# Kernel optimization log

Measured on AMD Instinct MI355X. Metric: run time of the kernel, lower is better.

The kernel has to match this reference:

```python
import jax, jax.numpy as jnp
import numpy as np

N = 32768        # nodes
E = 524288       # edges (avg degree 16)
F_NODE = 64      # NODE_FEATURE_DIM
H = 128          # GNN_HIDDEN
F_EDGE = 32      # EDGE_FEATURE_DIM
L = 3            # GNN_LAYERS
D = 256          # D_MODEL
B = 64           # graphs per batch
MAXN = N // B    # 512 nodes per graph (equal-size for static to_dense_batch)


def setup_inputs() -> dict:
    key = jax.random.key(0)
    ks = jax.random.split(key, 10)
    p = lambda k, shape: jax.random.normal(k, shape, jnp.float32) * 0.02
    return {
        "x": jax.random.normal(ks[0], (N, F_NODE), jnp.float32),
        "edge_attr": jax.random.normal(ks[1], (E, F_EDGE), jnp.float32),
        "node_emb_w": p(ks[2], (F_NODE, H)), "node_emb_b": jnp.zeros((H,), jnp.float32),
        "msg_w1": p(ks[3], (L, 2 * H + F_EDGE, 2 * H)), "msg_b1": jnp.zeros((L, 2 * H), jnp.float32),
        "msg_w2": p(ks[4], (L, 2 * H, H)), "msg_b2": jnp.zeros((L, H), jnp.float32),
        "upd_w": p(ks[5], (L, 2 * H, H)), "upd_b": jnp.zeros((L, H), jnp.float32),
        "upd_ln_g": jnp.ones((L, H), jnp.float32), "upd_ln_b": jnp.zeros((L, H), jnp.float32),
        "norm_g": jnp.ones((L, H), jnp.float32), "norm_b": jnp.zeros((L, H), jnp.float32),
        "proj_w": p(ks[6], (H, D)), "proj_b": jnp.zeros((D,), jnp.float32),
        "edge_index": jax.random.randint(ks[7], (2, E), 0, N),
        "batch": jnp.arange(N, dtype=jnp.int32) // MAXN,  # sorted, 64 graphs of 512
    }


def layer_norm(x, g, b, eps=1e-5):
    m = x.mean(-1, keepdims=True)
    v = ((x - m) ** 2).mean(-1, keepdims=True)
    return (x - m) * jax.lax.rsqrt(v + eps) * g + b


def reference(x, edge_attr, node_emb_w, node_emb_b, msg_w1, msg_b1, msg_w2, msg_b2,
              upd_w, upd_b, upd_ln_g, upd_ln_b, norm_g, norm_b, proj_w, proj_b,
              edge_index, batch):
    src, dst = edge_index[0], edge_index[1]  # PyG: x_j = x[src], x_i = x[dst]
    h = x @ node_emb_w + node_emb_b          # [N, H]
    n_layers = msg_w1.shape[0]
    for l in range(n_layers):
        # message: gather -> concat -> MLP (dropout inactive at eval)
        m = jnp.concatenate([h[dst], h[src], edge_attr], axis=-1)  # [E, 2H+Fe]
        m = jax.nn.relu(m @ msg_w1[l] + msg_b1[l])
        m = m @ msg_w2[l] + msg_b2[l]                               # [E, H]
        # aggregate: scatter-add over destination nodes
        aggr = jax.ops.segment_sum(m, dst, num_segments=h.shape[0])  # [N, H]
        # update: concat -> Linear -> ReLU -> LayerNorm
        u = jnp.concatenate([h, aggr], axis=-1) @ upd_w[l] + upd_b[l]
        u = layer_norm(jax.nn.relu(u), upd_ln_g[l], upd_ln_b[l])
        # residual + outer LayerNorm
        h = layer_norm(h + u, norm_g[l], norm_b[l])
    # to_dense_batch (batch sorted, equal-size graphs -> static [B, MAXN])
    n = h.shape[0]
    counts = jax.ops.segment_sum(jnp.ones((n,), jnp.int32), batch, num_segments=B)
    starts = jnp.concatenate([jnp.zeros((1,), jnp.int32), jnp.cumsum(counts)[:-1]])
    pos = jnp.arange(n, dtype=jnp.int32) - starts[batch]
    dense = jnp.zeros((B, MAXN, h.shape[-1]), h.dtype).at[batch, pos].set(h)
    mask = jnp.zeros((B, MAXN), bool).at[batch, pos].set(True)
    return dense @ proj_w + proj_b, mask
```

## Files before the change

### kernel.cpp

```cpp
#include <hip/hip_runtime.h>

#define NN 32768
#define NE 524288

typedef __attribute__((ext_vector_type(8))) short bf16x8;
typedef __attribute__((ext_vector_type(4))) float f32x4;

__device__ __forceinline__ unsigned short f2bf(float f) {
  unsigned int u = __float_as_uint(f);
  unsigned int r = (u + 0x7FFFu + ((u >> 16) & 1u)) >> 16;
  return (unsigned short)r;
}
__device__ __forceinline__ float bf2f(unsigned short s) {
  return __uint_as_float(((unsigned int)s) << 16);
}

__device__ __forceinline__ void lds_fence_wave() {
  asm volatile("s_waitcnt lgkmcnt(0)" ::: "memory");
  __builtin_amdgcn_sched_barrier(0);
}

__global__ void prep_frag_kernel(const float* __restrict__ W, int row0, int ldw, long lstrW,
                                 unsigned short* __restrict__ out, int outOff, int outLstr,
                                 int K, int N, int total) {
  int t = blockIdx.x * 256 + threadIdx.x;
  if (t >= total) return;
  int lane = t & 63, fi = t >> 6;
  int FR = (K >> 5) * (N >> 4);
  int l = fi / FR; fi -= l * FR;
  int NT = N >> 4;
  int nt = fi % NT, kc = fi / NT;
  int i = lane & 15, g = lane >> 4;
  const float* base = W + (long)l * lstrW;
  bf16x8 v;
#pragma unroll
  for (int j = 0; j < 8; ++j)
    v[j] = (short)f2bf(base[(long)(row0 + kc * 32 + g * 8 + j) * ldw + nt * 16 + i]);
  reinterpret_cast<bf16x8*>(out)[(long)(l * outLstr + outOff + fi) * 64 + lane] = v;
}

__global__ void wcomp_kernel(const float* __restrict__ W2, const float* __restrict__ Wu,
                             float* __restrict__ out) {
  int t = blockIdx.x * 256 + threadIdx.x;
  if (t >= 3 * 256 * 128) return;
  int c = t & 127, a = (t >> 7) & 255, l = t >> 15;
  const float* w2 = W2 + (long)l * 32768 + a * 128;
  const float* wu = Wu + (long)l * 32768 + 128 * 128 + c;
  float s = 0.f;
#pragma unroll 8
  for (int j = 0; j < 128; ++j) s += w2[j] * wu[j * 128];
  out[t] = s;
}

__global__ void c2_kernel(const float* __restrict__ b2, const float* __restrict__ Wu,
                          float* __restrict__ out) {
  int t = blockIdx.x * 256 + threadIdx.x;
  if (t >= 3 * 128) return;
  int c = t & 127, l = t >> 7;
  const float* bb = b2 + l * 128;
  const float* wu = Wu + (long)l * 32768 + 128 * 128 + c;
  float s = 0.f;
#pragma unroll 8
  for (int j = 0; j < 128; ++j) s += bb[j] * wu[j * 128];
  out[t] = s;
}

__global__ void hist_kernel(const int* __restrict__ eidx, int* __restrict__ deg) {
  int t = blockIdx.x * 256 + threadIdx.x;
  if (t < NE) atomicAdd(&deg[eidx[NE + t]], 1);
}

__global__ void scan_kernel(const int* __restrict__ deg, int* __restrict__ cursor,
                            float* __restrict__ degf) {
  __shared__ int lds[1024];
  int t = threadIdx.x;
  int vals[32];
  int s = 0;
#pragma unroll
  for (int j = 0; j < 32; ++j) {
    int d = deg[t * 32 + j];
    vals[j] = d; s += d;
    degf[t * 32 + j] = (float)d;
  }
  lds[t] = s;
  __syncthreads();
  for (int off = 1; off < 1024; off <<= 1) {
    int tmp = 0;
    if (t >= off) tmp = lds[t - off];
    __syncthreads();
    lds[t] += tmp;
    __syncthreads();
  }
  int run = lds[t] - s;
#pragma unroll
  for (int j = 0; j < 32; ++j) { cursor[t * 32 + j] = run; run += vals[j]; }
}

__global__ void scatter_kernel(const int* __restrict__ eidx, const float* __restrict__ ea,
                               int* __restrict__ cursor,
                               int* __restrict__ dsts, int* __restrict__ srcs,
                               unsigned short* __restrict__ ea_s) {
  int t = blockIdx.x * 256 + threadIdx.x;
  if (t >= NE) return;
  int d = eidx[NE + t], s = eidx[t];
  int pos = atomicAdd(&cursor[d], 1);
  dsts[pos] = d;
  srcs[pos] = s;
  const float4* ep = reinterpret_cast<const float4*>(ea + (long)t * 32);
  unsigned short* op = ea_s + (long)pos * 32;
#pragma unroll
  for (int q = 0; q < 4; ++q) {
    float4 f0 = ep[2 * q], f1 = ep[2 * q + 1];
    bf16x8 v;
    v[0] = (short)f2bf(f0.x); v[1] = (short)f2bf(f0.y);
    v[2] = (short)f2bf(f0.z); v[3] = (short)f2bf(f0.w);
    v[4] = (short)f2bf(f1.x); v[5] = (short)f2bf(f1.y);
    v[6] = (short)f2bf(f1.z); v[7] = (short)f2bf(f1.w);
    *reinterpret_cast<bf16x8*>(op + q * 8) = v;
  }
}

__global__ __launch_bounds__(256, 2)
void node_emb_kernel(const float* __restrict__ x,
                     const unsigned short* __restrict__ wf,
                     const float* __restrict__ bias,
                     unsigned short* __restrict__ h_bf,
                     float* __restrict__ h_f32) {
  int tid = threadIdx.x, lane = tid & 63, w = tid >> 6;
  int i = lane & 15, g = lane >> 4;
  int nbase = blockIdx.x * 64 + w * 16;
  f32x4 zero = {0.f, 0.f, 0.f, 0.f};
  f32x4 acc[8];
#pragma unroll
  for (int nt = 0; nt < 8; ++nt) acc[nt] = zero;
#pragma unroll
  for (int kc = 0; kc < 2; ++kc) {
    const float* xp = x + (nbase + i) * 64 + kc * 32 + g * 8;
    float4 f0 = *reinterpret_cast<const float4*>(xp);
    float4 f1 = *reinterpret_cast<const float4*>(xp + 4);
    bf16x8 af;
    af[0] = (short)f2bf(f0.x); af[1] = (short)f2bf(f0.y);
    af[2] = (short)f2bf(f0.z); af[3] = (short)f2bf(f0.w);
    af[4] = (short)f2bf(f1.x); af[5] = (short)f2bf(f1.y);
    af[6] = (short)f2bf(f1.z); af[7] = (short)f2bf(f1.w);
#pragma unroll
    for (int nt = 0; nt < 8; ++nt) {
      bf16x8 bf = reinterpret_cast<const bf16x8*>(wf)[(kc * 8 + nt) * 64 + lane];
      acc[nt] = __builtin_amdgcn_mfma_f32_16x16x32_bf16(af, bf, acc[nt], 0, 0, 0);
    }
  }
#pragma unroll
  for (int nt = 0; nt < 8; ++nt) {
    int c = nt * 16 + i;
    float b = bias[c];
#pragma unroll
    for (int r = 0; r < 4; ++r) {
      int node = nbase + 4 * g + r;
      float v = acc[nt][r] + b;
      h_f32[node * 128 + c] = v;
      h_bf[node * 128 + c] = f2bf(v);
    }
  }
}

__global__ __launch_bounds__(256, 2)
void pq_kernel(const unsigned short* __restrict__ h_bf,
               const unsigned short* __restrict__ wfa,
               const unsigned short* __restrict__ wfb,
               const float* __restrict__ b1,
               unsigned short* __restrict__ P, unsigned short* __restrict__ Q,
               float* __restrict__ haggr) {
  int tid = threadIdx.x, lane = tid & 63, w = tid >> 6;
  int i = lane & 15, g = lane >> 4;
  int nbase = blockIdx.x * 64 + w * 16;
  {
    const float4 zz = make_float4(0.f, 0.f, 0.f, 0.f);
    float4* hz = reinterpret_cast<float4*>(haggr + (long)blockIdx.x * 64 * 256);
#pragma unroll
    for (int it = 0; it < 16; ++it) hz[tid + 256 * it] = zz;
  }
  f32x4 zero = {0.f, 0.f, 0.f, 0.f};
  f32x4 accP[16], accQ[16];
#pragma unroll
  for (int nt = 0; nt < 16; ++nt) { accP[nt] = zero; accQ[nt] = zero; }
#pragma unroll
  for (int kc = 0; kc < 4; ++kc) {
    bf16x8 af = *reinterpret_cast<const bf16x8*>(h_bf + (nbase + i) * 128 + kc * 32 + g * 8);
#pragma unroll
    for (int nt = 0; nt < 16; ++nt) {
      bf16x8 ba = reinterpret_cast<const bf16x8*>(wfa)[(kc * 16 + nt) * 64 + lane];
      accP[nt] = __builtin_amdgcn_mfma_f32_16x16x32_bf16(af, ba, accP[nt], 0, 0, 0);
      bf16x8 bb = reinterpret_cast<const bf16x8*>(wfb)[(kc * 16 + nt) * 64 + lane];
      accQ[nt] = __builtin_amdgcn_mfma_f32_16x16x32_bf16(af, bb, accQ[nt], 0, 0, 0);
    }
  }
#pragma unroll
  for (int nt = 0; nt < 16; ++nt) {
    int c = nt * 16 + i;
    float b = b1[c];
#pragma unroll
    for (int r = 0; r < 4; ++r) {
      int node = nbase + 4 * g + r;
      P[(long)node * 256 + c] = f2bf(accP[nt][r] + b);
      Q[(long)node * 256 + c] = f2bf(accQ[nt][r]);
    }
  }
}

#define RP 264
__global__ __launch_bounds__(128, 4)
void edge_kernel5(const unsigned short* __restrict__ P,
                  const unsigned short* __restrict__ Q,
                  const int* __restrict__ dsts, const int* __restrict__ srcs,
                  const unsigned short* __restrict__ ea_s,
                  const unsigned short* __restrict__ w1cf,
                  float* __restrict__ haggr) {
  __shared__ unsigned short R[32 * RP];
  __shared__ float xch[2][256];
  const int tid = threadIdx.x;
  const int lane = tid & 63, w = tid >> 6;
  const int i = lane & 15, g = lane >> 4;
  const int p0 = blockIdx.x * 32;
  const int kb = w * 16;

  int dvs[16], svs[16];
#pragma unroll
  for (int k = 0; k < 16; ++k) {
    dvs[k] = __builtin_amdgcn_readfirstlane(dsts[p0 + kb + k]);
    svs[k] = __builtin_amdgcn_readfirstlane(srcs[p0 + kb + k]);
  }

  {
    bf16x8 bfrag = *reinterpret_cast<const bf16x8*>(ea_s + (long)(p0 + kb + i) * 32 + g * 8);
    f32x4 zero = {0.f, 0.f, 0.f, 0.f};
    f32x4 acc[16];
#pragma unroll
    for (int m = 0; m < 16; ++m) acc[m] = zero;
#pragma unroll
    for (int m = 0; m < 16; ++m) {
      bf16x8 afrag = reinterpret_cast<const bf16x8*>(w1cf)[m * 64 + lane];
      acc[m] = __builtin_amdgcn_mfma_f32_16x16x32_bf16(afrag, bfrag, acc[m], 0, 0, 0);
    }
#pragma unroll
    for (int m = 0; m < 16; ++m) {
      union { unsigned short s[4]; unsigned long long u; } pk;
#pragma unroll
      for (int r = 0; r < 4; ++r) pk.s[r] = f2bf(acc[m][r]);
      *reinterpret_cast<unsigned long long*>(&R[(kb + i) * RP + m * 16 + 4 * g]) = pk.u;
    }
  }

  const int c4 = lane * 4;
  ushort4 qv[16];
#pragma unroll
  for (int k = 0; k < 16; ++k)
    qv[k] = *reinterpret_cast<const ushort4*>(Q + (long)svs[k] * 256 + c4);
  float pf[4];
  int dvPrev = dvs[0];
  {
    ushort4 pv = *reinterpret_cast<const ushort4*>(P + (long)dvPrev * 256 + c4);
    pf[0] = bf2f(pv.x); pf[1] = bf2f(pv.y); pf[2] = bf2f(pv.z); pf[3] = bf2f(pv.w);
  }

  lds_fence_wave();

  float acc4[4] = {0.f, 0.f, 0.f, 0.f};
#pragma unroll
  for (int k = 0; k < 16; ++k) {
    int dv = dvs[k];
    if (dv != dvPrev) {
      *reinterpret_cast<float4*>(&xch[w][c4]) = make_float4(acc4[0], acc4[1], acc4[2], acc4[3]);
      lds_fence_wave();
      float* hp = haggr + (long)dvPrev * 256;
#pragma unroll
      for (int j = 0; j < 4; ++j) atomicAdd(hp + lane + 64 * j, xch[w][lane + 64 * j]);
      acc4[0] = acc4[1] = acc4[2] = acc4[3] = 0.f;
      ushort4 pv = *reinterpret_cast<const ushort4*>(P + (long)dv * 256 + c4);
      pf[0] = bf2f(pv.x); pf[1] = bf2f(pv.y); pf[2] = bf2f(pv.z); pf[3] = bf2f(pv.w);
      dvPrev = dv;
    }
    ushort4 rv = *reinterpret_cast<const ushort4*>(&R[(kb + k) * RP + c4]);
    float v0 = pf[0] + bf2f(qv[k].x) + bf2f(rv.x);
    float v1 = pf[1] + bf2f(qv[k].y) + bf2f(rv.y);
    float v2 = pf[2] + bf2f(qv[k].z) + bf2f(rv.z);
    float v3 = pf[3] + bf2f(qv[k].w) + bf2f(rv.w);
    acc4[0] += v0 > 0.f ? v0 : 0.f;
    acc4[1] += v1 > 0.f ? v1 : 0.f;
    acc4[2] += v2 > 0.f ? v2 : 0.f;
    acc4[3] += v3 > 0.f ? v3 : 0.f;
  }
  {
    *reinterpret_cast<float4*>(&xch[w][c4]) = make_float4(acc4[0], acc4[1], acc4[2], acc4[3]);
    lds_fence_wave();
    float* hp = haggr + (long)dvPrev * 256;
#pragma unroll
    for (int j = 0; j < 4; ++j) atomicAdd(hp + lane + 64 * j, xch[w][lane + 64 * j]);
  }
}

__global__ __launch_bounds__(256, 2)
void upd_kernel2(const unsigned short* __restrict__ h_bf_in,
                 float* __restrict__ h_f32,
                 const float* __restrict__ haggr,
                 const float* __restrict__ degf,
                 const unsigned short* __restrict__ wf,
                 const float* __restrict__ ub, const float* __restrict__ c2,
                 const float* __restrict__ g1, const float* __restrict__ be1,
                 const float* __restrict__ g2, const float* __restrict__ be2,
                 unsigned short* __restrict__ h_bf_out) {
  int tid = threadIdx.x, lane = tid & 63, w = tid >> 6;
  int i = lane & 15, g = lane >> 4;
  int nbase = blockIdx.x * 64 + w * 16;
  f32x4 zero = {0.f, 0.f, 0.f, 0.f};
  f32x4 acc[8];
#pragma unroll
  for (int nt = 0; nt < 8; ++nt) acc[nt] = zero;
#pragma unroll
  for (int kc = 0; kc < 12; ++kc) {
    bf16x8 af;
    if (kc < 4) {
      af = *reinterpret_cast<const bf16x8*>(h_bf_in + (nbase + i) * 128 + kc * 32 + g * 8);
    } else {
      const float* ap = haggr + (long)(nbase + i) * 256 + (kc - 4) * 32 + g * 8;
      float4 f0 = *reinterpret_cast<const float4*>(ap);
      float4 f1 = *reinterpret_cast<const float4*>(ap + 4);
      af[0] = (short)f2bf(f0.x); af[1] = (short)f2bf(f0.y);
      af[2] = (short)f2bf(f0.z); af[3] = (short)f2bf(f0.w);
      af[4] = (short)f2bf(f1.x); af[5] = (short)f2bf(f1.y);
      af[6] = (short)f2bf(f1.z); af[7] = (short)f2bf(f1.w);
    }
#pragma unroll
    for (int nt = 0; nt < 8; ++nt) {
      bf16x8 bf = reinterpret_cast<const bf16x8*>(wf)[(kc * 8 + nt) * 64 + lane];
      acc[nt] = __builtin_amdgcn_mfma_f32_16x16x32_bf16(af, bf, acc[nt], 0, 0, 0);
    }
  }
  float vv[8][4];
#pragma unroll
  for (int nt = 0; nt < 8; ++nt) {
    int c = nt * 16 + i;
    float b = ub[c], cc = c2[c];
#pragma unroll
    for (int r = 0; r < 4; ++r) {
      int node = nbase + 4 * g + r;
      float t = acc[nt][r] + b + degf[node] * cc;
      vv[nt][r] = t > 0.f ? t : 0.f;
    }
  }
#pragma unroll
  for (int r = 0; r < 4; ++r) {
    float s = 0.f, s2 = 0.f;
#pragma unroll
    for (int nt = 0; nt < 8; ++nt) { s += vv[nt][r]; s2 += vv[nt][r] * vv[nt][r]; }
#pragma unroll
    for (int mk = 1; mk < 16; mk <<= 1) { s += __shfl_xor(s, mk, 64); s2 += __shfl_xor(s2, mk, 64); }
    float mean = s * (1.f / 128.f);
    float var = s2 * (1.f / 128.f) - mean * mean;
    float inv = rsqrtf(var + 1e-5f);
    int node = nbase + 4 * g + r;
    float tv[8];
    float sb = 0.f, sb2 = 0.f;
#pragma unroll
    for (int nt = 0; nt < 8; ++nt) {
      int c = nt * 16 + i;
      float u = (vv[nt][r] - mean) * inv * g1[c] + be1[c];
      float t = h_f32[node * 128 + c] + u;
      tv[nt] = t;
      sb += t; sb2 += t * t;
    }
#pragma unroll
    for (int mk = 1; mk < 16; mk <<= 1) { sb += __shfl_xor(sb, mk, 64); sb2 += __shfl_xor(sb2, mk, 64); }
    float mean2 = sb * (1.f / 128.f);
    float var2 = sb2 * (1.f / 128.f) - mean2 * mean2;
    float inv2 = rsqrtf(var2 + 1e-5f);
#pragma unroll
    for (int nt = 0; nt < 8; ++nt) {
      int c = nt * 16 + i;
      float o = (tv[nt] - mean2) * inv2 * g2[c] + be2[c];
      h_f32[node * 128 + c] = o;
      h_bf_out[node * 128 + c] = f2bf(o);
    }
  }
}

__global__ __launch_bounds__(256, 2)
void proj_kernel(const unsigned short* __restrict__ h_bf,
                 const unsigned short* __restrict__ wf,
                 const float* __restrict__ bias,
                 float* __restrict__ out, float* __restrict__ mask) {
  int tid = threadIdx.x, lane = tid & 63, w = tid >> 6;
  int i = lane & 15, g = lane >> 4;
  int nbase = blockIdx.x * 64 + w * 16;
  if (tid < 64) mask[blockIdx.x * 64 + tid] = 1.0f;
  f32x4 zero = {0.f, 0.f, 0.f, 0.f};
  f32x4 acc[16];
#pragma unroll
  for (int nt = 0; nt < 16; ++nt) acc[nt] = zero;
#pragma unroll
  for (int kc = 0; kc < 4; ++kc) {
    bf16x8 af = *reinterpret_cast<const bf16x8*>(h_bf + (nbase + i) * 128 + kc * 32 + g * 8);
#pragma unroll
    for (int nt = 0; nt < 16; ++nt) {
      bf16x8 bf = reinterpret_cast<const bf16x8*>(wf)[(kc * 16 + nt) * 64 + lane];
      acc[nt] = __builtin_amdgcn_mfma_f32_16x16x32_bf16(af, bf, acc[nt], 0, 0, 0);
    }
  }
#pragma unroll
  for (int nt = 0; nt < 16; ++nt) {
    int c = nt * 16 + i;
    float b = bias[c];
#pragma unroll
    for (int r = 0; r < 4; ++r) {
      int node = nbase + 4 * g + r;
      out[(long)node * 256 + c] = acc[nt][r] + b;
    }
  }
}

extern "C" void kernel_launch(void* const* d_in, const int* in_sizes, int n_in,
                              void* d_out, int out_size, void* d_ws, size_t ws_size,
                              hipStream_t stream) {
  const float* x      = (const float*)d_in[0];
  const float* ea     = (const float*)d_in[1];
  const float* emb_w  = (const float*)d_in[2];
  const float* emb_b  = (const float*)d_in[3];
  const float* msg_w1 = (const float*)d_in[4];
  const float* msg_b1 = (const float*)d_in[5];
  const float* msg_w2 = (const float*)d_in[6];
  const float* msg_b2 = (const float*)d_in[7];
  const float* upd_w  = (const float*)d_in[8];
  const float* upd_b  = (const float*)d_in[9];
  const float* uln_g  = (const float*)d_in[10];
  const float* uln_b  = (const float*)d_in[11];
  const float* nrm_g  = (const float*)d_in[12];
  const float* nrm_b  = (const float*)d_in[13];
  const float* proj_w = (const float*)d_in[14];
  const float* proj_b = (const float*)d_in[15];
  const int*   eidx   = (const int*)d_in[16];

  char* ws = (char*)d_ws;
  size_t off = 0;
  auto take = [&](size_t b) { char* p = ws + off; off = (off + b + 255) & ~(size_t)255; return p; };
  unsigned short* h_bf  = (unsigned short*)take((size_t)NN * 128 * 2);
  float*          h_f32 = (float*)take((size_t)NN * 128 * 4);
  unsigned short* Pb    = (unsigned short*)take((size_t)NN * 256 * 2);
  unsigned short* Qb    = (unsigned short*)take((size_t)NN * 256 * 2);
  float*          haggr = (float*)take((size_t)NN * 256 * 4);
  unsigned short* ea_s  = (unsigned short*)take((size_t)NE * 32 * 2);
  int*            dsts  = (int*)take((size_t)NE * 4);
  int*            srcs  = (int*)take((size_t)NE * 4);
  int*            deg   = (int*)take((size_t)NN * 4);
  int*            cursor= (int*)take((size_t)NN * 4);
  float*          degf  = (float*)take((size_t)NN * 4);
  float*          wcomp = (float*)take((size_t)3 * 256 * 128 * 4);
  float*          c2b   = (float*)take((size_t)3 * 128 * 4);
  unsigned short* wembf = (unsigned short*)take((size_t)16 * 64 * 8 * 2);
  unsigned short* w1af  = (unsigned short*)take((size_t)3 * 64 * 64 * 8 * 2);
  unsigned short* w1bf  = (unsigned short*)take((size_t)3 * 64 * 64 * 8 * 2);
  unsigned short* w1cf  = (unsigned short*)take((size_t)3 * 16 * 64 * 8 * 2);
  unsigned short* wupdf = (unsigned short*)take((size_t)3 * 96 * 64 * 8 * 2);
  unsigned short* wprojf= (unsigned short*)take((size_t)64 * 64 * 8 * 2);
  (void)ws_size; (void)n_in; (void)in_sizes;

  hipMemsetAsync(deg, 0, (size_t)NN * 4, stream);
  hist_kernel<<<2048, 256, 0, stream>>>(eidx, deg);
  scan_kernel<<<1, 1024, 0, stream>>>(deg, cursor, degf);
  scatter_kernel<<<2048, 256, 0, stream>>>(eidx, ea, cursor, dsts, srcs, ea_s);
  wcomp_kernel<<<384, 256, 0, stream>>>(msg_w2, upd_w, wcomp);
  c2_kernel<<<2, 256, 0, stream>>>(msg_b2, upd_w, c2b);
  prep_frag_kernel<<<4, 256, 0, stream>>>(emb_w, 0, 128, 0, wembf, 0, 16, 64, 128, 1024);
  prep_frag_kernel<<<48, 256, 0, stream>>>(msg_w1, 0, 256, 73728, w1af, 0, 64, 128, 256, 12288);
  prep_frag_kernel<<<48, 256, 0, stream>>>(msg_w1, 128, 256, 73728, w1bf, 0, 64, 128, 256, 12288);
  prep_frag_kernel<<<12, 256, 0, stream>>>(msg_w1, 256, 256, 73728, w1cf, 0, 16, 32, 256, 3072);
  prep_frag_kernel<<<24, 256, 0, stream>>>(upd_w, 0, 128, 32768, wupdf, 0, 96, 128, 128, 6144);
  prep_frag_kernel<<<48, 256, 0, stream>>>(wcomp, 0, 128, 32768, wupdf, 32, 96, 256, 128, 12288);
  prep_frag_kernel<<<16, 256, 0, stream>>>(proj_w, 0, 256, 0, wprojf, 0, 64, 128, 256, 4096);

  node_emb_kernel<<<512, 256, 0, stream>>>(x, wembf, emb_b, h_bf, h_f32);

  for (int l = 0; l < 3; ++l) {
    pq_kernel<<<512, 256, 0, stream>>>(h_bf, w1af + (size_t)l * 32768, w1bf + (size_t)l * 32768,
                                       msg_b1 + l * 256, Pb, Qb, haggr);
    edge_kernel5<<<NE / 32, 128, 0, stream>>>(Pb, Qb, dsts, srcs, ea_s,
                                              w1cf + (size_t)l * 8192, haggr);
    upd_kernel2<<<512, 256, 0, stream>>>(h_bf, h_f32, haggr, degf,
                                         wupdf + (size_t)l * 49152, upd_b + l * 128,
                                         c2b + l * 128,
                                         uln_g + l * 128, uln_b + l * 128,
                                         nrm_g + l * 128, nrm_b + l * 128, h_bf);
  }

  proj_kernel<<<512, 256, 0, stream>>>(h_bf, wprojf, proj_b, (float*)d_out,
                                       (float*)d_out + (size_t)NN * 256);
}
```

Baseline: 505.3 us.

## Batch weight-prep launches, swizzle edge blocks, and prefetch all P rows

Merges the seven prep_frag launches into one prep_all kernel and folds c2_kernel into wcomp_kernel, cutting launch overhead. In the edge kernel, block indices are swizzled across eight groups to spread concurrently running blocks over the edge range. All 16 P rows are loaded up front alongside the Q rows instead of lazily on destination change, so more loads are in flight. The cost is more registers and redundant P loads, since sorted edges often share a destination.

Measured after the change: 501.4 us. About the same (-0.8%).

```diff
diff --git a/kernel.cpp b/kernel.cpp
--- a/kernel.cpp
+++ b/kernel.cpp
@@ -20,10 +20,10 @@
   __builtin_amdgcn_sched_barrier(0);
 }
 
-__global__ void prep_frag_kernel(const float* __restrict__ W, int row0, int ldw, long lstrW,
-                                 unsigned short* __restrict__ out, int outOff, int outLstr,
-                                 int K, int N, int total) {
-  int t = blockIdx.x * 256 + threadIdx.x;
+__device__ __forceinline__ void prep_frag_body(
+    const float* __restrict__ W, int row0, int ldw, long lstrW,
+    unsigned short* __restrict__ out, int outOff, int outLstr,
+    int K, int N, int t, int total) {
   if (t >= total) return;
   int lane = t & 63, fi = t >> 6;
   int FR = (K >> 5) * (N >> 4);
@@ -39,30 +39,51 @@
   reinterpret_cast<bf16x8*>(out)[(long)(l * outLstr + outOff + fi) * 64 + lane] = v;
 }
 
+__global__ void prep_all_kernel(const float* __restrict__ emb_w,
+                                const float* __restrict__ msg_w1,
+                                const float* __restrict__ upd_w,
+                                const float* __restrict__ wcomp,
+                                const float* __restrict__ proj_w,
+                                unsigned short* __restrict__ wembf,
+                                unsigned short* __restrict__ w1af,
+                                unsigned short* __restrict__ w1bf,
+                                unsigned short* __restrict__ w1cf,
+                                unsigned short* __restrict__ wupdf,
+                                unsigned short* __restrict__ wprojf) {
+  int b = blockIdx.x, tid = threadIdx.x;
+  if (b < 4)        prep_frag_body(emb_w,  0,   128, 0,     wembf,  0,  16, 64,  128, b * 256 + tid, 1024);
+  else if (b < 52)  prep_frag_body(msg_w1, 0,   256, 73728, w1af,   0,  64, 128, 256, (b - 4) * 256 + tid, 12288);
+  else if (b < 100) prep_frag_body(msg_w1, 128, 256, 73728, w1bf,   0,  64, 128, 256, (b - 52) * 256 + tid, 12288);
+  else if (b < 112) prep_frag_body(msg_w1, 256, 256, 73728, w1cf,   0,  16, 32,  256, (b - 100) * 256 + tid, 3072);
+  else if (b < 136) prep_frag_body(upd_w,  0,   128, 32768, wupdf,  0,  96, 128, 128, (b - 112) * 256 + tid, 6144);
+  else if (b < 184) prep_frag_body(wcomp,  0,   128, 32768, wupdf,  32, 96, 256, 128, (b - 136) * 256 + tid, 12288);
+  else              prep_frag_body(proj_w, 0,   256, 0,     wprojf, 0,  64, 128, 256, (b - 184) * 256 + tid, 4096);
+}
+
 __global__ void wcomp_kernel(const float* __restrict__ W2, const float* __restrict__ Wu,
-                             float* __restrict__ out) {
+                             const float* __restrict__ b2,
+                             float* __restrict__ out, float* __restrict__ c2out) {
   int t = blockIdx.x * 256 + threadIdx.x;
-  if (t >= 3 * 256 * 128) return;
-  int c = t & 127, a = (t >> 7) & 255, l = t >> 15;
-  const float* w2 = W2 + (long)l * 32768 + a * 128;
-  const float* wu = Wu + (long)l * 32768 + 128 * 128 + c;
-  float s = 0.f;
+  if (t < 3 * 256 * 128) {
+    int c = t & 127, a = (t >> 7) & 255, l = t >> 15;
+    const float* w2 = W2 + (long)l * 32768 + a * 128;
+    const float* wu = Wu + (long)l * 32768 + 128 * 128 + c;
+    float s = 0.f;
 #pragma unroll 8
-  for (int j = 0; j < 128; ++j) s += w2[j] * wu[j * 128];
-  out[t] = s;
-}
-
-__global__ void c2_kernel(const float* __restrict__ b2, const float* __restrict__ Wu,
-                          float* __restrict__ out) {
-  int t = blockIdx.x * 256 + threadIdx.x;
-  if (t >= 3 * 128) return;
-  int c = t & 127, l = t >> 7;
-  const float* bb = b2 + l * 128;
-  const float* wu = Wu + (long)l * 32768 + 128 * 128 + c;
-  float s = 0.f;
+    for (int j = 0; j < 128; ++j) s += w2[j] * wu[j * 128];
+    out[t] = s;
+  } else {
+    int t2 = t - 3 * 256 * 128;
+    if (t2 < 3 * 128) {
+      int c = t2 & 127, l = t2 >> 7;
+      const float* bb = b2 + l * 128;
+      const float* wu = Wu + (long)l * 32768 + 128 * 128 + c;
+      float s = 0.f;
 #pragma unroll 8
-  for (int j = 0; j < 128; ++j) s += bb[j] * wu[j * 128];
-  out[t] = s;
+      for (int j = 0; j < 128; ++j) s += bb[j] * wu[j * 128];
+      c2out[t2] = s;
+    }
+  }
 }
 
 __global__ void hist_kernel(const int* __restrict__ eidx, int* __restrict__ deg) {
@@ -209,7 +230,7 @@
 
 #define RP 264
 __global__ __launch_bounds__(128, 4)
-void edge_kernel5(const unsigned short* __restrict__ P,
+void edge_kernel6(const unsigned short* __restrict__ P,
                   const unsigned short* __restrict__ Q,
                   const int* __restrict__ dsts, const int* __restrict__ srcs,
                   const unsigned short* __restrict__ ea_s,
@@ -220,7 +241,9 @@
   const int tid = threadIdx.x;
   const int lane = tid & 63, w = tid >> 6;
   const int i = lane & 15, g = lane >> 4;
-  const int p0 = blockIdx.x * 32;
+  const int bid = blockIdx.x;
+  const int swz = (bid & 7) * 2048 + (bid >> 3);
+  const int p0 = swz * 32;
   const int kb = w * 16;
 
   int dvs[16], svs[16];
@@ -251,20 +274,17 @@
   }
 
   const int c4 = lane * 4;
-  ushort4 qv[16];
-#pragma unroll
-  for (int k = 0; k < 16; ++k)
+  ushort4 qv[16], pv[16];
+#pragma unroll
+  for (int k = 0; k < 16; ++k) {
     qv[k] = *reinterpret_cast<const ushort4*>(Q + (long)svs[k] * 256 + c4);
-  float pf[4];
+    pv[k] = *reinterpret_cast<const ushort4*>(P + (long)dvs[k] * 256 + c4);
+  }
+
+  lds_fence_wave();
+
+  float acc4[4] = {0.f, 0.f, 0.f, 0.f};
   int dvPrev = dvs[0];
-  {
-    ushort4 pv = *reinterpret_cast<const ushort4*>(P + (long)dvPrev * 256 + c4);
-    pf[0] = bf2f(pv.x); pf[1] = bf2f(pv.y); pf[2] = bf2f(pv.z); pf[3] = bf2f(pv.w);
-  }
-
-  lds_fence_wave();
-
-  float acc4[4] = {0.f, 0.f, 0.f, 0.f};
 #pragma unroll
   for (int k = 0; k < 16; ++k) {
     int dv = dvs[k];
@@ -275,15 +295,13 @@
 #pragma unroll
       for (int j = 0; j < 4; ++j) atomicAdd(hp + lane + 64 * j, xch[w][lane + 64 * j]);
       acc4[0] = acc4[1] = acc4[2] = acc4[3] = 0.f;
-      ushort4 pv = *reinterpret_cast<const ushort4*>(P + (long)dv * 256 + c4);
-      pf[0] = bf2f(pv.x); pf[1] = bf2f(pv.y); pf[2] = bf2f(pv.z); pf[3] = bf2f(pv.w);
       dvPrev = dv;
     }
     ushort4 rv = *reinterpret_cast<const ushort4*>(&R[(kb + k) * RP + c4]);
-    float v0 = pf[0] + bf2f(qv[k].x) + bf2f(rv.x);
-    float v1 = pf[1] + bf2f(qv[k].y) + bf2f(rv.y);
-    float v2 = pf[2] + bf2f(qv[k].z) + bf2f(rv.z);
-    float v3 = pf[3] + bf2f(qv[k].w) + bf2f(rv.w);
+    float v0 = bf2f(pv[k].x) + bf2f(qv[k].x) + bf2f(rv.x);
+    float v1 = bf2f(pv[k].y) + bf2f(qv[k].y) + bf2f(rv.y);
+    float v2 = bf2f(pv[k].z) + bf2f(qv[k].z) + bf2f(rv.z);
+    float v3 = bf2f(pv[k].w) + bf2f(qv[k].w) + bf2f(rv.w);
     acc4[0] += v0 > 0.f ? v0 : 0.f;
     acc4[1] += v1 > 0.f ? v1 : 0.f;
     acc4[2] += v2 > 0.f ? v2 : 0.f;
@@ -466,22 +484,16 @@
   hist_kernel<<<2048, 256, 0, stream>>>(eidx, deg);
   scan_kernel<<<1, 1024, 0, stream>>>(deg, cursor, degf);
   scatter_kernel<<<2048, 256, 0, stream>>>(eidx, ea, cursor, dsts, srcs, ea_s);
-  wcomp_kernel<<<384, 256, 0, stream>>>(msg_w2, upd_w, wcomp);
-  c2_kernel<<<2, 256, 0, stream>>>(msg_b2, upd_w, c2b);
-  prep_frag_kernel<<<4, 256, 0, stream>>>(emb_w, 0, 128, 0, wembf, 0, 16, 64, 128, 1024);
-  prep_frag_kernel<<<48, 256, 0, stream>>>(msg_w1, 0, 256, 73728, w1af, 0, 64, 128, 256, 12288);
-  prep_frag_kernel<<<48, 256, 0, stream>>>(msg_w1, 128, 256, 73728, w1bf, 0, 64, 128, 256, 12288);
-  prep_frag_kernel<<<12, 256, 0, stream>>>(msg_w1, 256, 256, 73728, w1cf, 0, 16, 32, 256, 3072);
-  prep_frag_kernel<<<24, 256, 0, stream>>>(upd_w, 0, 128, 32768, wupdf, 0, 96, 128, 128, 6144);
-  prep_frag_kernel<<<48, 256, 0, stream>>>(wcomp, 0, 128, 32768, wupdf, 32, 96, 256, 128, 12288);
-  prep_frag_kernel<<<16, 256, 0, stream>>>(proj_w, 0, 256, 0, wprojf, 0, 64, 128, 256, 4096);
+  wcomp_kernel<<<386, 256, 0, stream>>>(msg_w2, upd_w, msg_b2, wcomp, c2b);
+  prep_all_kernel<<<200, 256, 0, stream>>>(emb_w, msg_w1, upd_w, wcomp, proj_w,
+                                           wembf, w1af, w1bf, w1cf, wupdf, wprojf);
 
   node_emb_kernel<<<512, 256, 0, stream>>>(x, wembf, emb_b, h_bf, h_f32);
 
   for (int l = 0; l < 3; ++l) {
     pq_kernel<<<512, 256, 0, stream>>>(h_bf, w1af + (size_t)l * 32768, w1bf + (size_t)l * 32768,
                                        msg_b1 + l * 256, Pb, Qb, haggr);
-    edge_kernel5<<<NE / 32, 128, 0, stream>>>(Pb, Qb, dsts, srcs, ea_s,
+    edge_kernel6<<<NE / 32, 128, 0, stream>>>(Pb, Qb, dsts, srcs, ea_s,
                                               w1cf + (size_t)l * 8192, haggr);
     upd_kernel2<<<512, 256, 0, stream>>>(h_bf, h_f32, haggr, degf,
                                          wupdf + (size_t)l * 49152, upd_b + l * 128,
```
